# Optimization experiments

Hardware: AMD Instinct MI355X
Metric: run time of the kernel (lower is better)

## Reference

```python
import jax, jax.numpy as jnp
import numpy as np

N_NODES = 50000
N_EDGES = 800000
D_IN = 16


def gcn_conv(x, edge_index, W, b, n_nodes):
    """PyG GCNConv: x' = D^{-1/2} (A + I) D^{-1/2} X W + b (add_self_loops=True)."""
    h = x @ W  # [N, d_out] - transform before propagate (small d => cheaper)
    src = jnp.concatenate([edge_index[0], jnp.arange(n_nodes)])  # add self-loops
    dst = jnp.concatenate([edge_index[1], jnp.arange(n_nodes)])
    deg = jax.ops.segment_sum(jnp.ones_like(dst, dtype=h.dtype), dst,
                              num_segments=n_nodes)  # in-degree incl. self-loop
    deg_inv_sqrt = jnp.where(deg > 0, jax.lax.rsqrt(deg), 0.0)
    norm = deg_inv_sqrt[src] * deg_inv_sqrt[dst]  # [E+N]
    msg = h[src] * norm[:, None]                  # gather + scale
    out = jax.ops.segment_sum(msg, dst, num_segments=n_nodes)  # scatter-add
    return out + b


def setup_inputs() -> dict:
    key = jax.random.key(0)
    ks = jax.random.split(key, 16)
    d = D_IN
    x = jax.random.normal(ks[0], (N_NODES, d), dtype=jnp.float32)
    edge_index = jax.random.randint(ks[1], (2, N_EDGES), 0, N_NODES, dtype=jnp.int64)

    def glorot(k, fan_in, fan_out):
        s = (6.0 / (fan_in + fan_out)) ** 0.5
        return jax.random.uniform(k, (fan_in, fan_out), jnp.float32, -s, s)

    return {
        "x": x,
        "edge_index": edge_index,
        "W1": glorot(ks[2], d, 2 * d),      "b1": jnp.zeros((2 * d,), jnp.float32),
        "W2": glorot(ks[3], 2 * d, 4 * d),  "b2": jnp.zeros((4 * d,), jnp.float32),
        "W3": glorot(ks[4], 4 * d, 8 * d),  "b3": jnp.zeros((8 * d,), jnp.float32),
        "Wl1": glorot(ks[5], 8 * d, 4 * d), "bl1": jnp.zeros((4 * d,), jnp.float32),
        "Wl2": glorot(ks[6], 4 * d, 2 * d), "bl2": jnp.zeros((2 * d,), jnp.float32),
        "Wl3": glorot(ks[7], 2 * d, d),     "bl3": jnp.zeros((d,), jnp.float32),
    }


def reference(x, edge_index, W1, b1, W2, b2, W3, b3, Wl1, bl1, Wl2, bl2, Wl3, bl3):
    n = x.shape[0]
    # note: original applies relu twice per conv; relu is idempotent
    out = jax.nn.relu(gcn_conv(x, edge_index, W1, b1, n))
    out = jax.nn.relu(gcn_conv(out, edge_index, W2, b2, n))
    out = jax.nn.relu(gcn_conv(out, edge_index, W3, b3, n))
    out = jax.nn.relu(out @ Wl1 + bl1)
    out = jax.nn.relu(out @ Wl2 + bl2)
    out = jax.nn.relu(out @ Wl3 + bl3)
    return out
```

## Files before the change

### kernel.cpp

```cpp
#include <hip/hip_runtime.h>

#define TPB 256
#define TE  2048
#define MAXB 6144

typedef _Float16 half_t;
typedef _Float16 half4 __attribute__((ext_vector_type(4)));
typedef _Float16 half8 __attribute__((ext_vector_type(8)));
typedef float float8v __attribute__((ext_vector_type(8)));

static inline int cdiv(int a, int b) { return (a + b - 1) / b; }


__global__ void __launch_bounds__(TPB)
k_binscatter(const int* __restrict__ src, const int* __restrict__ dst,
             int* __restrict__ bcur, int* __restrict__ ncnt,
             unsigned int* __restrict__ gbuf, int e, int nb) {
    __shared__ int lcnt[256], loffs[256], lcur[256], gres[256];
    __shared__ int ss[256];
    __shared__ unsigned int ldata[TE];
    const int tid = threadIdx.x;
    const int base = blockIdx.x * TE;
    const int cnt = min(TE, e - base);
    lcnt[tid] = 0;
    __syncthreads();

    unsigned int myv[TE / TPB];
    int myb[TE / TPB];
#pragma unroll
    for (int k = 0; k < TE / TPB; ++k) {
        int j = tid + k * TPB;
        if (j < cnt) {
            int d = dst[base + j], s = src[base + j];
            int b = d >> 8;
            myv[k] = ((unsigned)b << 24) | ((unsigned)(d & 255) << 16) | (unsigned)s;
            myb[k] = b;
            atomicAdd(&lcnt[b], 1);
            atomicAdd(&ncnt[d], 1);
        } else myb[k] = -1;
    }
    __syncthreads();
    {
        int v = lcnt[tid];
        ss[tid] = v;
        __syncthreads();
        for (int d = 1; d < 256; d <<= 1) {
            int x2 = (tid >= d) ? ss[tid - d] : 0;
            __syncthreads();
            ss[tid] += x2;
            __syncthreads();
        }
        loffs[tid] = ss[tid] - v;
        lcur[tid] = ss[tid] - v;
    }
    __syncthreads();
    if (tid < nb && lcnt[tid])
        gres[tid] = tid * MAXB + atomicAdd(&bcur[tid], lcnt[tid]);
#pragma unroll
    for (int k = 0; k < TE / TPB; ++k) {
        if (myb[k] >= 0) {
            int p = atomicAdd(&lcur[myb[k]], 1);
            ldata[p] = myv[k];
        }
    }
    __syncthreads();
    for (int j = tid; j < cnt; j += TPB) {
        unsigned int v = ldata[j];
        int b = v >> 24;
        gbuf[gres[b] + (j - loffs[b])] = v & 0xFFFFFFu;
    }
}

__global__ void __launch_bounds__(TPB)
k_csr(const unsigned int* __restrict__ gbuf, const int* __restrict__ bcur,
      const int* __restrict__ ncnt, const float* __restrict__ x,
      int* __restrict__ offs, unsigned short* __restrict__ nch,
      float* __restrict__ dinv, unsigned short* __restrict__ ssrc,
      half_t* __restrict__ G, int n, int nb) {
    __shared__ int ss[256], lcur2[256];
    __shared__ float sdinv[256];
    __shared__ unsigned short stage[MAXB];
    const int b = blockIdx.x;
    const int t = threadIdx.x;
    const int s0 = b * MAXB;
    const int m = bcur[b];

    const int v = ncnt[b * 256 + t];
    const int pv = (v + 7) & ~7;
    ss[t] = pv;
    __syncthreads();
    for (int d = 1; d < 256; d <<= 1) {
        int x2 = (t >= d) ? ss[t - d] : 0;
        __syncthreads();
        ss[t] += x2;
        __syncthreads();
    }
    const int lo = ss[t] - pv;
    lcur2[t] = lo;
    float di = rsqrtf((float)v + 1.0f);
    sdinv[t] = di;
    int node = b * 256 + t;
    if (node < n) {
        offs[node] = s0 + lo;
        nch[node] = (unsigned short)(pv >> 3);
        dinv[node] = di;
    }
    __syncthreads();
    for (int j = t; j < m; j += TPB) {
        unsigned int u = gbuf[s0 + j];
        int p = atomicAdd(&lcur2[(u >> 16) & 255], 1);
        stage[p] = (unsigned short)(u & 0xFFFFu);
    }
    __syncthreads();
    for (int q = lo + v; q < lo + pv; ++q)
        stage[q] = (unsigned short)n;
    __syncthreads();
    const int tot = ss[255];
    for (int j = t; j < tot; j += TPB) ssrc[s0 + j] = stage[j];

    const int base = b * 256;
    const int cn = min(256, n - base);
    const float4* X4 = (const float4*)x;
    half4* G4 = (half4*)G;
    for (int j = t; j < cn * 4; j += TPB) {
        int nl = j >> 2, k4 = j & 3;
        float4 vv = X4[(size_t)(base + nl) * 4 + k4];
        float d = sdinv[nl];
        half4 h;
        h.x = (half_t)(vv.x * d); h.y = (half_t)(vv.y * d);
        h.z = (half_t)(vv.z * d); h.w = (half_t)(vv.w * d);
        G4[(size_t)(base + nl) * 4 + k4] = h;
    }
    if (b == 0 && t < 4) G4[(size_t)n * 4 + t] = half4{0, 0, 0, 0};
}

template<int DI, int DO, int R, bool SCALE, bool OUT_HALF, bool WHALF, bool ZSENT>
__global__ void __launch_bounds__(TPB, 4)
k_conv(const int* __restrict__ offs, const unsigned short* __restrict__ nch,
       const unsigned short* __restrict__ ssrc,
       const half_t* __restrict__ G, const float* __restrict__ dinv,
       const float* __restrict__ W, const float* __restrict__ b,
       void* __restrict__ outp, int n) {
    constexpr int CT = DO / 4;
    constexpr int RT = TPB / CT;
    constexpr int TM = RT * R;
    constexpr int K4 = DI / 4;
    constexpr int PX = K4 + 1;
    constexpr int C  = DI / 8;
    static_assert(TM * C == TPB, "gather/gemm tile mismatch");
    __shared__ float4 sW4[WHALF ? 1 : DI * CT];
    __shared__ half4  sWh[WHALF ? DI * CT : 1];
    __shared__ float4 sX4[TM * PX];
    __shared__ int soffs[TM];
    __shared__ unsigned short snch[TM];
    const int tid = threadIdx.x;
    const int r0 = blockIdx.x * TM;

    const float4* Wg = (const float4*)W;
    for (int t = tid; t < DI * CT; t += TPB) {
        float4 w = Wg[t];
        if (WHALF) {
            half4 h;
            h.x = (half_t)w.x; h.y = (half_t)w.y;
            h.z = (half_t)w.z; h.w = (half_t)w.w;
            sWh[t] = h;
        } else {
            sW4[t] = w;
        }
    }
    if (tid < TM) {
        int row = r0 + tid;
        soffs[tid] = (row < n) ? offs[row] : 0;
        snch[tid] = (row < n) ? nch[row] : (unsigned short)0;
    }
    __syncthreads();

    {
        int lrow = tid / C;
        int gc = tid - lrow * C;
        int row = r0 + lrow;
        float8v acc;
#pragma unroll
        for (int q = 0; q < 8; ++q) acc[q] = 0.f;
        if (row < n) {
            const half8* Grow = (const half8*)G;
            const unsigned gcU = (unsigned)gc;
            half8 hs = Grow[(unsigned)row * C + gcU];
#pragma unroll
            for (int q = 0; q < 8; ++q) acc[q] = (float)hs[q];
            const int nchunks = snch[lrow];
            const uint4* sv = (const uint4*)(ssrc + soffs[lrow]);
            int k = 0;
            for (; k + 2 <= nchunks; k += 2) {
                uint4 pa = sv[k];
                uint4 pb = sv[k + 1];
                unsigned a0 = pa.x & 0xFFFFu, a1 = pa.x >> 16;
                unsigned a2 = pa.y & 0xFFFFu, a3 = pa.y >> 16;
                unsigned a4 = pa.z & 0xFFFFu, a5 = pa.z >> 16;
                unsigned a6 = pa.w & 0xFFFFu, a7 = pa.w >> 16;
                unsigned b0 = pb.x & 0xFFFFu, b1 = pb.x >> 16;
                unsigned b2 = pb.y & 0xFFFFu, b3 = pb.y >> 16;
                unsigned b4 = pb.z & 0xFFFFu, b5 = pb.z >> 16;
                unsigned b6 = pb.w & 0xFFFFu, b7 = pb.w >> 16;
                half8 ga0 = Grow[a0 * C + gcU];
                half8 ga1 = Grow[a1 * C + gcU];
                half8 ga2 = Grow[a2 * C + gcU];
                half8 ga3 = Grow[a3 * C + gcU];
                half8 ga4 = Grow[a4 * C + gcU];
                half8 ga5 = Grow[a5 * C + gcU];
                half8 ga6 = Grow[a6 * C + gcU];
                half8 ga7 = Grow[a7 * C + gcU];
                half8 gb0 = Grow[b0 * C + gcU];
                half8 gb1 = Grow[b1 * C + gcU];
                half8 gb2 = Grow[b2 * C + gcU];
                half8 gb3 = Grow[b3 * C + gcU];
                half8 gb4 = Grow[b4 * C + gcU];
                half8 gb5 = Grow[b5 * C + gcU];
                half8 gb6 = Grow[b6 * C + gcU];
                half8 gb7 = Grow[b7 * C + gcU];
#pragma unroll
                for (int q = 0; q < 8; ++q)
                    acc[q] += (((((float)ga0[q] + (float)ga1[q]) + ((float)ga2[q] + (float)ga3[q]))
                             +  (((float)ga4[q] + (float)ga5[q]) + ((float)ga6[q] + (float)ga7[q])))
                             + ((((float)gb0[q] + (float)gb1[q]) + ((float)gb2[q] + (float)gb3[q]))
                             +  (((float)gb4[q] + (float)gb5[q]) + ((float)gb6[q] + (float)gb7[q]))));
            }
            if (k < nchunks) {
                uint4 pk = sv[k];
                unsigned a0 = pk.x & 0xFFFFu, a1 = pk.x >> 16;
                unsigned a2 = pk.y & 0xFFFFu, a3 = pk.y >> 16;
                unsigned a4 = pk.z & 0xFFFFu, a5 = pk.z >> 16;
                unsigned a6 = pk.w & 0xFFFFu, a7 = pk.w >> 16;
                half8 g0 = Grow[a0 * C + gcU];
                half8 g1 = Grow[a1 * C + gcU];
                half8 g2 = Grow[a2 * C + gcU];
                half8 g3 = Grow[a3 * C + gcU];
                half8 g4 = Grow[a4 * C + gcU];
                half8 g5 = Grow[a5 * C + gcU];
                half8 g6 = Grow[a6 * C + gcU];
                half8 g7 = Grow[a7 * C + gcU];
#pragma unroll
                for (int q = 0; q < 8; ++q)
                    acc[q] += (((float)g0[q] + (float)g1[q]) + ((float)g2[q] + (float)g3[q]))
                            + (((float)g4[q] + (float)g5[q]) + ((float)g6[q] + (float)g7[q]));
            }
            float di = dinv[row];
#pragma unroll
            for (int q = 0; q < 8; ++q) acc[q] *= di;
        }
        sX4[lrow * PX + 2 * gc]     = make_float4(acc[0], acc[1], acc[2], acc[3]);
        sX4[lrow * PX + 2 * gc + 1] = make_float4(acc[4], acc[5], acc[6], acc[7]);
    }
    __syncthreads();

    const int c = tid & (CT - 1);
    const int rg = tid / CT;
    const int rbase = rg * R;
    float4 acc[R];
#pragma unroll
    for (int r = 0; r < R; ++r) acc[r] = make_float4(0.f, 0.f, 0.f, 0.f);
#pragma unroll 2
    for (int k4 = 0; k4 < K4; ++k4) {
        float4 xv[R];
#pragma unroll
        for (int r = 0; r < R; ++r) xv[r] = sX4[(rbase + r) * PX + k4];
#pragma unroll
        for (int kk = 0; kk < 4; ++kk) {
            float4 wv;
            if (WHALF) {
                half4 wh = sWh[(k4 * 4 + kk) * CT + c];
                wv = make_float4((float)wh.x, (float)wh.y, (float)wh.z, (float)wh.w);
            } else {
                wv = sW4[(k4 * 4 + kk) * CT + c];
            }
#pragma unroll
            for (int r = 0; r < R; ++r) {
                float xs = (kk == 0) ? xv[r].x : (kk == 1) ? xv[r].y
                         : (kk == 2) ? xv[r].z : xv[r].w;
                acc[r].x += xs * wv.x; acc[r].y += xs * wv.y;
                acc[r].z += xs * wv.z; acc[r].w += xs * wv.w;
            }
        }
    }

    float4 bc = ((const float4*)b)[c];
#pragma unroll
    for (int r = 0; r < R; ++r) {
        int row = r0 + rbase + r;
        if (row < n) {
            float4 o;
            o.x = fmaxf(acc[r].x + bc.x, 0.f);
            o.y = fmaxf(acc[r].y + bc.y, 0.f);
            o.z = fmaxf(acc[r].z + bc.z, 0.f);
            o.w = fmaxf(acc[r].w + bc.w, 0.f);
            if (SCALE) {
                float d = dinv[row];
                o.x *= d; o.y *= d; o.z *= d; o.w *= d;
            }
            if (OUT_HALF) {
                half4 h;
                h.x = (half_t)o.x; h.y = (half_t)o.y;
                h.z = (half_t)o.z; h.w = (half_t)o.w;
                ((half4*)outp)[(size_t)row * CT + c] = h;
            } else {
                ((float4*)outp)[(size_t)row * CT + c] = o;
            }
        }
    }
    if (ZSENT && OUT_HALF && blockIdx.x == 0 && tid < CT)
        ((half4*)outp)[(size_t)n * CT + tid] = half4{0, 0, 0, 0};
}

__global__ void __launch_bounds__(TPB, 4)
k_conv3_head(const int* __restrict__ offs, const unsigned short* __restrict__ nch,
             const unsigned short* __restrict__ ssrc,
             const half_t* __restrict__ G, const float* __restrict__ dinv,
             const float* __restrict__ W, const float* __restrict__ b,
             const float* __restrict__ Wl1, const float* __restrict__ bl1,
             const float* __restrict__ Wl2, const float* __restrict__ bl2,
             const float* __restrict__ Wl3, const float* __restrict__ bl3,
             float* __restrict__ out, int n) {
    constexpr int DI = 64, DO = 128, R = 4;
    constexpr int CT = DO / 4;
    constexpr int TM = (TPB / CT) * R;
    constexpr int K4 = DI / 4;
    constexpr int PX = K4 + 1;
    constexpr int C  = DI / 8;
    constexpr int XP = 136;
    __shared__ union {
        struct { half4 sWh[DI * CT]; float4 sX4[TM * PX]; } g;
        struct { half_t X3[TM * XP]; half_t hW1[128 * 64];
                 float h1[TM * 65]; float h2[TM * 33]; } h;
    } S;
    __shared__ int soffs[TM];
    __shared__ unsigned short snch[TM];
    const int tid = threadIdx.x;
    const int r0 = blockIdx.x * TM;

    const float4* Wg = (const float4*)W;
    for (int t = tid; t < DI * CT; t += TPB) {
        float4 w = Wg[t];
        half4 hh;
        hh.x = (half_t)w.x; hh.y = (half_t)w.y;
        hh.z = (half_t)w.z; hh.w = (half_t)w.w;
        S.g.sWh[t] = hh;
    }
    if (tid < TM) {
        int row = r0 + tid;
        soffs[tid] = (row < n) ? offs[row] : 0;
        snch[tid] = (row < n) ? nch[row] : (unsigned short)0;
    }
    __syncthreads();

    {
        int lrow = tid / C;
        int gc = tid - lrow * C;
        int row = r0 + lrow;
        float8v acc;
#pragma unroll
        for (int q = 0; q < 8; ++q) acc[q] = 0.f;
        if (row < n) {
            const half8* Grow = (const half8*)G;
            const unsigned gcU = (unsigned)gc;
            half8 hs = Grow[(unsigned)row * C + gcU];
#pragma unroll
            for (int q = 0; q < 8; ++q) acc[q] = (float)hs[q];
            const int nchunks = snch[lrow];
            const uint4* sv = (const uint4*)(ssrc + soffs[lrow]);
            int k = 0;
            for (; k + 2 <= nchunks; k += 2) {
                uint4 pa = sv[k];
                uint4 pb = sv[k + 1];
                unsigned a0 = pa.x & 0xFFFFu, a1 = pa.x >> 16;
                unsigned a2 = pa.y & 0xFFFFu, a3 = pa.y >> 16;
                unsigned a4 = pa.z & 0xFFFFu, a5 = pa.z >> 16;
                unsigned a6 = pa.w & 0xFFFFu, a7 = pa.w >> 16;
                unsigned b0 = pb.x & 0xFFFFu, b1 = pb.x >> 16;
                unsigned b2 = pb.y & 0xFFFFu, b3 = pb.y >> 16;
                unsigned b4 = pb.z & 0xFFFFu, b5 = pb.z >> 16;
                unsigned b6 = pb.w & 0xFFFFu, b7 = pb.w >> 16;
                half8 ga0 = Grow[a0 * C + gcU];
                half8 ga1 = Grow[a1 * C + gcU];
                half8 ga2 = Grow[a2 * C + gcU];
                half8 ga3 = Grow[a3 * C + gcU];
                half8 ga4 = Grow[a4 * C + gcU];
                half8 ga5 = Grow[a5 * C + gcU];
                half8 ga6 = Grow[a6 * C + gcU];
                half8 ga7 = Grow[a7 * C + gcU];
                half8 gb0 = Grow[b0 * C + gcU];
                half8 gb1 = Grow[b1 * C + gcU];
                half8 gb2 = Grow[b2 * C + gcU];
                half8 gb3 = Grow[b3 * C + gcU];
                half8 gb4 = Grow[b4 * C + gcU];
                half8 gb5 = Grow[b5 * C + gcU];
                half8 gb6 = Grow[b6 * C + gcU];
                half8 gb7 = Grow[b7 * C + gcU];
#pragma unroll
                for (int q = 0; q < 8; ++q)
                    acc[q] += (((((float)ga0[q] + (float)ga1[q]) + ((float)ga2[q] + (float)ga3[q]))
                             +  (((float)ga4[q] + (float)ga5[q]) + ((float)ga6[q] + (float)ga7[q])))
                             + ((((float)gb0[q] + (float)gb1[q]) + ((float)gb2[q] + (float)gb3[q]))
                             +  (((float)gb4[q] + (float)gb5[q]) + ((float)gb6[q] + (float)gb7[q]))));
            }
            if (k < nchunks) {
                uint4 pk = sv[k];
                unsigned a0 = pk.x & 0xFFFFu, a1 = pk.x >> 16;
                unsigned a2 = pk.y & 0xFFFFu, a3 = pk.y >> 16;
                unsigned a4 = pk.z & 0xFFFFu, a5 = pk.z >> 16;
                unsigned a6 = pk.w & 0xFFFFu, a7 = pk.w >> 16;
                half8 g0 = Grow[a0 * C + gcU];
                half8 g1 = Grow[a1 * C + gcU];
                half8 g2 = Grow[a2 * C + gcU];
                half8 g3 = Grow[a3 * C + gcU];
                half8 g4 = Grow[a4 * C + gcU];
                half8 g5 = Grow[a5 * C + gcU];
                half8 g6 = Grow[a6 * C + gcU];
                half8 g7 = Grow[a7 * C + gcU];
#pragma unroll
                for (int q = 0; q < 8; ++q)
                    acc[q] += (((float)g0[q] + (float)g1[q]) + ((float)g2[q] + (float)g3[q]))
                            + (((float)g4[q] + (float)g5[q]) + ((float)g6[q] + (float)g7[q]));
            }
            float di = dinv[row];
#pragma unroll
            for (int q = 0; q < 8; ++q) acc[q] *= di;
        }
        S.g.sX4[lrow * PX + 2 * gc]     = make_float4(acc[0], acc[1], acc[2], acc[3]);
        S.g.sX4[lrow * PX + 2 * gc + 1] = make_float4(acc[4], acc[5], acc[6], acc[7]);
    }
    __syncthreads();

    const int c = tid & (CT - 1);
    const int rg = tid / CT;
    const int rbase = rg * R;
    float4 acc[R];
#pragma unroll
    for (int r = 0; r < R; ++r) acc[r] = make_float4(0.f, 0.f, 0.f, 0.f);
#pragma unroll 2
    for (int k4 = 0; k4 < K4; ++k4) {
        float4 xv[R];
#pragma unroll
        for (int r = 0; r < R; ++r) xv[r] = S.g.sX4[(rbase + r) * PX + k4];
#pragma unroll
        for (int kk = 0; kk < 4; ++kk) {
            half4 wh = S.g.sWh[(k4 * 4 + kk) * CT + c];
            float4 wv = make_float4((float)wh.x, (float)wh.y, (float)wh.z, (float)wh.w);
#pragma unroll
            for (int r = 0; r < R; ++r) {
                float xs = (kk == 0) ? xv[r].x : (kk == 1) ? xv[r].y
                         : (kk == 2) ? xv[r].z : xv[r].w;
                acc[r].x += xs * wv.x; acc[r].y += xs * wv.y;
                acc[r].z += xs * wv.z; acc[r].w += xs * wv.w;
            }
        }
    }
    {
        float4 bc = ((const float4*)b)[c];
#pragma unroll
        for (int r = 0; r < R; ++r) {
            acc[r].x = fmaxf(acc[r].x + bc.x, 0.f);
            acc[r].y = fmaxf(acc[r].y + bc.y, 0.f);
            acc[r].z = fmaxf(acc[r].z + bc.z, 0.f);
            acc[r].w = fmaxf(acc[r].w + bc.w, 0.f);
        }
    }
    __syncthreads();

#pragma unroll
    for (int r = 0; r < R; ++r) {
        half4 hv;
        hv.x = (half_t)acc[r].x; hv.y = (half_t)acc[r].y;
        hv.z = (half_t)acc[r].z; hv.w = (half_t)acc[r].w;
        *(half4*)&S.h.X3[(rbase + r) * XP + c * 4] = hv;
    }
    for (int t = tid; t < 128 * 64; t += TPB) S.h.hW1[t] = (half_t)Wl1[t];
    __syncthreads();

    {
        const int c4 = tid & 15;
        const int rowg = tid >> 4;
        float a1[2][4];
#pragma unroll
        for (int r = 0; r < 2; ++r)
#pragma unroll
            for (int j = 0; j < 4; ++j) a1[r][j] = 0.f;
        for (int k8 = 0; k8 < 16; ++k8) {
            half8 xh[2];
#pragma unroll
            for (int r = 0; r < 2; ++r)
                xh[r] = *(const half8*)&S.h.X3[(rowg * 2 + r) * XP + k8 * 8];
#pragma unroll
            for (int q = 0; q < 8; ++q) {
                int k = k8 * 8 + q;
                half4 w = *(const half4*)&S.h.hW1[k * 64 + c4 * 4];
                float w0 = (float)w.x, w1 = (float)w.y, w2 = (float)w.z, w3 = (float)w.w;
#pragma unroll
                for (int r = 0; r < 2; ++r) {
                    float xs = (float)xh[r][q];
                    a1[r][0] += xs * w0; a1[r][1] += xs * w1;
                    a1[r][2] += xs * w2; a1[r][3] += xs * w3;
                }
            }
        }
        float4 bc = ((const float4*)bl1)[c4];
#pragma unroll
        for (int r = 0; r < 2; ++r) {
            int rl = rowg * 2 + r;
            S.h.h1[rl * 65 + c4 * 4 + 0] = fmaxf(a1[r][0] + bc.x, 0.f);
            S.h.h1[rl * 65 + c4 * 4 + 1] = fmaxf(a1[r][1] + bc.y, 0.f);
            S.h.h1[rl * 65 + c4 * 4 + 2] = fmaxf(a1[r][2] + bc.z, 0.f);
            S.h.h1[rl * 65 + c4 * 4 + 3] = fmaxf(a1[r][3] + bc.w, 0.f);
        }
    }
    __syncthreads();

    {
        const int c4 = tid & 7;
        const int rl = tid >> 3;
        float a2[4] = {0.f, 0.f, 0.f, 0.f};
#pragma unroll 4
        for (int k = 0; k < 64; ++k) {
            float4 w = ((const float4*)Wl2)[k * 8 + c4];
            float xs = S.h.h1[rl * 65 + k];
            a2[0] += xs * w.x; a2[1] += xs * w.y;
            a2[2] += xs * w.z; a2[3] += xs * w.w;
        }
        float4 bc = ((const float4*)bl2)[c4];
        S.h.h2[rl * 33 + c4 * 4 + 0] = fmaxf(a2[0] + bc.x, 0.f);
        S.h.h2[rl * 33 + c4 * 4 + 1] = fmaxf(a2[1] + bc.y, 0.f);
        S.h.h2[rl * 33 + c4 * 4 + 2] = fmaxf(a2[2] + bc.z, 0.f);
        S.h.h2[rl * 33 + c4 * 4 + 3] = fmaxf(a2[3] + bc.w, 0.f);
    }
    __syncthreads();

    {
        const int c4 = tid & 3;
        const int rl = tid >> 2;
        if (rl < TM) {
            float s0 = 0.f, s1 = 0.f, s2 = 0.f, s3 = 0.f;
#pragma unroll 4
            for (int k = 0; k < 32; ++k) {
                float4 w = ((const float4*)Wl3)[k * 4 + c4];
                float xs = S.h.h2[rl * 33 + k];
                s0 += xs * w.x; s1 += xs * w.y;
                s2 += xs * w.z; s3 += xs * w.w;
            }
            int row = r0 + rl;
            if (row < n) {
                float4 bc = ((const float4*)bl3)[c4];
                float4 o;
                o.x = fmaxf(s0 + bc.x, 0.f);
                o.y = fmaxf(s1 + bc.y, 0.f);
                o.z = fmaxf(s2 + bc.z, 0.f);
                o.w = fmaxf(s3 + bc.w, 0.f);
                ((float4*)out)[(size_t)row * 4 + c4] = o;
            }
        }
    }
}

extern "C" void kernel_launch(void* const* d_in, const int* in_sizes, int n_in,
                              void* d_out, int out_size, void* d_ws, size_t ws_size,
                              hipStream_t stream) {
    const float* x   = (const float*)d_in[0];
    const int*   ei  = (const int*)d_in[1];
    const float* W1  = (const float*)d_in[2];
    const float* bb1 = (const float*)d_in[3];
    const float* W2  = (const float*)d_in[4];
    const float* bb2 = (const float*)d_in[5];
    const float* W3  = (const float*)d_in[6];
    const float* bb3 = (const float*)d_in[7];
    const float* Wl1 = (const float*)d_in[8];
    const float* bl1 = (const float*)d_in[9];
    const float* Wl2 = (const float*)d_in[10];
    const float* bl2 = (const float*)d_in[11];
    const float* Wl3 = (const float*)d_in[12];
    const float* bl3 = (const float*)d_in[13];
    float* out = (float*)d_out;

    const int n = in_sizes[0] / 16;
    const int e = in_sizes[1] / 2;
    const int* src = ei;
    const int* dst = ei + e;
    const int nb = cdiv(n, 256);

    char* p = (char*)d_ws;
    auto alloc = [&](size_t bytes) {
        char* r = p;
        p += (bytes + 255) & ~(size_t)255;
        return r;
    };
    int*            bcur = (int*)           alloc(1024);
    int*            ncnt = (int*)           alloc((size_t)nb * 256 * 4);
    float*          dinv = (float*)         alloc((size_t)n * 4);
    int*            offs = (int*)           alloc((size_t)n * 4);
    unsigned short* nch  = (unsigned short*)alloc((size_t)n * 2);
    unsigned int*   gbuf = (unsigned int*)  alloc((size_t)nb * MAXB * 4);
    unsigned short* ssrc = (unsigned short*)alloc((size_t)nb * MAXB * 2);
    half_t*         H1   = (half_t*)        alloc((size_t)(n + 1) * 64 * 2);
    half_t*         H2   = (half_t*)        alloc((size_t)(n + 1) * 32 * 2);

    hipMemsetAsync(bcur, 0, 1024 + (size_t)nb * 256 * 4, stream);
    k_binscatter<<<cdiv(e, TE), TPB, 0, stream>>>(src, dst, bcur, ncnt, gbuf, e, nb);
    k_csr<<<nb, TPB, 0, stream>>>(gbuf, bcur, ncnt, x, offs, nch, dinv, ssrc, H1, n, nb);

    k_conv<16, 32, 4, true, true, false, true><<<cdiv(n, 128), TPB, 0, stream>>>(
        offs, nch, ssrc, H1, dinv, W1, bb1, H2, n);
    k_conv<32, 64, 4, true, true, false, true><<<cdiv(n, 64), TPB, 0, stream>>>(
        offs, nch, ssrc, H2, dinv, W2, bb2, H1, n);
    k_conv3_head<<<cdiv(n, 32), TPB, 0, stream>>>(
        offs, nch, ssrc, H1, dinv, W3, bb3, Wl1, bl1, Wl2, bl2, Wl3, bl3, out, n);
}
```

Baseline: 218.2 us.

## Use MFMA f16 matrix cores for conv3 transform and first head layer

Replaces the scalar FMA dense products in the fused conv3+head kernel (the 64->128 conv3 weight multiply and the 128->64 Wl1 layer) with 16x16x32 f16 MFMA instructions. Weights are transposed into padded shared-memory tiles and the aggregated features are stored as f16. The kernel now handles 32 rows per block instead of 32 with the old R scheme. The aim is to cut ALU time in the head. It adds a transpose-on-load with scattered 16-bit shared stores, and rounds the conv3 inputs to f16 before the multiply.

```diff
diff --git a/kernel.cpp b/kernel.cpp
--- a/kernel.cpp
+++ b/kernel.cpp
@@ -8,6 +8,7 @@
 typedef _Float16 half4 __attribute__((ext_vector_type(4)));
 typedef _Float16 half8 __attribute__((ext_vector_type(8)));
 typedef float float8v __attribute__((ext_vector_type(8)));
+typedef float f32x4 __attribute__((ext_vector_type(4)));
 
 static inline int cdiv(int a, int b) { return (a + b - 1) / b; }
 
@@ -320,30 +321,34 @@
              const float* __restrict__ Wl2, const float* __restrict__ bl2,
              const float* __restrict__ Wl3, const float* __restrict__ bl3,
              float* __restrict__ out, int n) {
-    constexpr int DI = 64, DO = 128, R = 4;
-    constexpr int CT = DO / 4;
-    constexpr int TM = (TPB / CT) * R;
-    constexpr int K4 = DI / 4;
-    constexpr int PX = K4 + 1;
-    constexpr int C  = DI / 8;
-    constexpr int XP = 136;
-    __shared__ union {
-        struct { half4 sWh[DI * CT]; float4 sX4[TM * PX]; } g;
-        struct { half_t X3[TM * XP]; half_t hW1[128 * 64];
+    constexpr int TM = 32;
+    constexpr int C  = 8;
+    constexpr int XPA = 72;
+    constexpr int XPB = 136;
+    __shared__ __align__(16) union {
+        struct { half_t sWhT[128 * XPA]; half_t X16[TM * XPA]; } g;
+        struct { half_t X3[TM * XPB]; half_t sW1T[64 * XPB];
                  float h1[TM * 65]; float h2[TM * 33]; } h;
     } S;
     __shared__ int soffs[TM];
     __shared__ unsigned short snch[TM];
     const int tid = threadIdx.x;
     const int r0 = blockIdx.x * TM;
-
-    const float4* Wg = (const float4*)W;
-    for (int t = tid; t < DI * CT; t += TPB) {
-        float4 w = Wg[t];
-        half4 hh;
-        hh.x = (half_t)w.x; hh.y = (half_t)w.y;
-        hh.z = (half_t)w.z; hh.w = (half_t)w.w;
-        S.g.sWh[t] = hh;
+    const int lane = tid & 63;
+    const int wv = tid >> 6;
+    const int lr = lane & 15;
+    const int kq = lane >> 4;
+
+    {
+        const float4* Wg = (const float4*)W;
+        for (int t = tid; t < 64 * 32; t += TPB) {
+            int k = t >> 5, c4 = t & 31;
+            float4 w = Wg[t];
+            S.g.sWhT[(c4 * 4 + 0) * XPA + k] = (half_t)w.x;
+            S.g.sWhT[(c4 * 4 + 1) * XPA + k] = (half_t)w.y;
+            S.g.sWhT[(c4 * 4 + 2) * XPA + k] = (half_t)w.z;
+            S.g.sWhT[(c4 * 4 + 3) * XPA + k] = (half_t)w.w;
+        }
     }
     if (tid < TM) {
         int row = r0 + tid;
@@ -425,92 +430,76 @@
 #pragma unroll
             for (int q = 0; q < 8; ++q) acc[q] *= di;
         }
-        S.g.sX4[lrow * PX + 2 * gc]     = make_float4(acc[0], acc[1], acc[2], acc[3]);
-        S.g.sX4[lrow * PX + 2 * gc + 1] = make_float4(acc[4], acc[5], acc[6], acc[7]);
-    }
-    __syncthreads();
-
-    const int c = tid & (CT - 1);
-    const int rg = tid / CT;
-    const int rbase = rg * R;
-    float4 acc[R];
-#pragma unroll
-    for (int r = 0; r < R; ++r) acc[r] = make_float4(0.f, 0.f, 0.f, 0.f);
-#pragma unroll 2
-    for (int k4 = 0; k4 < K4; ++k4) {
-        float4 xv[R];
-#pragma unroll
-        for (int r = 0; r < R; ++r) xv[r] = S.g.sX4[(rbase + r) * PX + k4];
-#pragma unroll
-        for (int kk = 0; kk < 4; ++kk) {
-            half4 wh = S.g.sWh[(k4 * 4 + kk) * CT + c];
-            float4 wv = make_float4((float)wh.x, (float)wh.y, (float)wh.z, (float)wh.w);
-#pragma unroll
-            for (int r = 0; r < R; ++r) {
-                float xs = (kk == 0) ? xv[r].x : (kk == 1) ? xv[r].y
-                         : (kk == 2) ? xv[r].z : xv[r].w;
-                acc[r].x += xs * wv.x; acc[r].y += xs * wv.y;
-                acc[r].z += xs * wv.z; acc[r].w += xs * wv.w;
-            }
-        }
-    }
-    {
-        float4 bc = ((const float4*)b)[c];
-#pragma unroll
-        for (int r = 0; r < R; ++r) {
-            acc[r].x = fmaxf(acc[r].x + bc.x, 0.f);
-            acc[r].y = fmaxf(acc[r].y + bc.y, 0.f);
-            acc[r].z = fmaxf(acc[r].z + bc.z, 0.f);
-            acc[r].w = fmaxf(acc[r].w + bc.w, 0.f);
-        }
-    }
-    __syncthreads();
-
-#pragma unroll
-    for (int r = 0; r < R; ++r) {
-        half4 hv;
-        hv.x = (half_t)acc[r].x; hv.y = (half_t)acc[r].y;
-        hv.z = (half_t)acc[r].z; hv.w = (half_t)acc[r].w;
-        *(half4*)&S.h.X3[(rbase + r) * XP + c * 4] = hv;
-    }
-    for (int t = tid; t < 128 * 64; t += TPB) S.h.hW1[t] = (half_t)Wl1[t];
-    __syncthreads();
-
-    {
-        const int c4 = tid & 15;
-        const int rowg = tid >> 4;
-        float a1[2][4];
-#pragma unroll
-        for (int r = 0; r < 2; ++r)
-#pragma unroll
-            for (int j = 0; j < 4; ++j) a1[r][j] = 0.f;
-        for (int k8 = 0; k8 < 16; ++k8) {
-            half8 xh[2];
-#pragma unroll
-            for (int r = 0; r < 2; ++r)
-                xh[r] = *(const half8*)&S.h.X3[(rowg * 2 + r) * XP + k8 * 8];
-#pragma unroll
-            for (int q = 0; q < 8; ++q) {
-                int k = k8 * 8 + q;
-                half4 w = *(const half4*)&S.h.hW1[k * 64 + c4 * 4];
-                float w0 = (float)w.x, w1 = (float)w.y, w2 = (float)w.z, w3 = (float)w.w;
-#pragma unroll
-                for (int r = 0; r < 2; ++r) {
-                    float xs = (float)xh[r][q];
-                    a1[r][0] += xs * w0; a1[r][1] += xs * w1;
-                    a1[r][2] += xs * w2; a1[r][3] += xs * w3;
-                }
-            }
-        }
-        float4 bc = ((const float4*)bl1)[c4];
-#pragma unroll
-        for (int r = 0; r < 2; ++r) {
-            int rl = rowg * 2 + r;
-            S.h.h1[rl * 65 + c4 * 4 + 0] = fmaxf(a1[r][0] + bc.x, 0.f);
-            S.h.h1[rl * 65 + c4 * 4 + 1] = fmaxf(a1[r][1] + bc.y, 0.f);
-            S.h.h1[rl * 65 + c4 * 4 + 2] = fmaxf(a1[r][2] + bc.z, 0.f);
-            S.h.h1[rl * 65 + c4 * 4 + 3] = fmaxf(a1[r][3] + bc.w, 0.f);
-        }
+        half8 hv;
+#pragma unroll
+        for (int q = 0; q < 8; ++q) hv[q] = (half_t)acc[q];
+        *(half8*)&S.g.X16[lrow * XPA + gc * 8] = hv;
+    }
+    __syncthreads();
+
+    f32x4 acc3[2][2];
+#pragma unroll
+    for (int mt = 0; mt < 2; ++mt)
+#pragma unroll
+        for (int nt = 0; nt < 2; ++nt) acc3[mt][nt] = f32x4{0.f, 0.f, 0.f, 0.f};
+#pragma unroll
+    for (int ks = 0; ks < 2; ++ks) {
+        half8 a0 = *(const half8*)&S.g.X16[lr * XPA + ks * 32 + kq * 8];
+        half8 a1 = *(const half8*)&S.g.X16[(lr + 16) * XPA + ks * 32 + kq * 8];
+        half8 b0 = *(const half8*)&S.g.sWhT[(wv * 32 + lr) * XPA + ks * 32 + kq * 8];
+        half8 b1 = *(const half8*)&S.g.sWhT[(wv * 32 + 16 + lr) * XPA + ks * 32 + kq * 8];
+        acc3[0][0] = __builtin_amdgcn_mfma_f32_16x16x32_f16(a0, b0, acc3[0][0], 0, 0, 0);
+        acc3[0][1] = __builtin_amdgcn_mfma_f32_16x16x32_f16(a0, b1, acc3[0][1], 0, 0, 0);
+        acc3[1][0] = __builtin_amdgcn_mfma_f32_16x16x32_f16(a1, b0, acc3[1][0], 0, 0, 0);
+        acc3[1][1] = __builtin_amdgcn_mfma_f32_16x16x32_f16(a1, b1, acc3[1][1], 0, 0, 0);
+    }
+    const float bc30 = b[wv * 32 + lr];
+    const float bc31 = b[wv * 32 + 16 + lr];
+    __syncthreads();
+
+#pragma unroll
+    for (int mt = 0; mt < 2; ++mt)
+#pragma unroll
+        for (int nt = 0; nt < 2; ++nt) {
+            float bb = nt ? bc31 : bc30;
+#pragma unroll
+            for (int j = 0; j < 4; ++j) {
+                float v = fmaxf(acc3[mt][nt][j] + bb, 0.f);
+                S.h.X3[(mt * 16 + kq * 4 + j) * XPB + wv * 32 + nt * 16 + lr] = (half_t)v;
+            }
+        }
+    {
+        const float4* W1g = (const float4*)Wl1;
+        for (int t = tid; t < 128 * 16; t += TPB) {
+            int k = t >> 4, c4 = t & 15;
+            float4 w = W1g[t];
+            S.h.sW1T[(c4 * 4 + 0) * XPB + k] = (half_t)w.x;
+            S.h.sW1T[(c4 * 4 + 1) * XPB + k] = (half_t)w.y;
+            S.h.sW1T[(c4 * 4 + 2) * XPB + k] = (half_t)w.z;
+            S.h.sW1T[(c4 * 4 + 3) * XPB + k] = (half_t)w.w;
+        }
+    }
+    __syncthreads();
+
+    f32x4 h1a[2];
+    h1a[0] = f32x4{0.f, 0.f, 0.f, 0.f};
+    h1a[1] = f32x4{0.f, 0.f, 0.f, 0.f};
+#pragma unroll
+    for (int ks = 0; ks < 4; ++ks) {
+        half8 a0 = *(const half8*)&S.h.X3[lr * XPB + ks * 32 + kq * 8];
+        half8 a1 = *(const half8*)&S.h.X3[(lr + 16) * XPB + ks * 32 + kq * 8];
+        half8 bb = *(const half8*)&S.h.sW1T[(wv * 16 + lr) * XPB + ks * 32 + kq * 8];
+        h1a[0] = __builtin_amdgcn_mfma_f32_16x16x32_f16(a0, bb, h1a[0], 0, 0, 0);
+        h1a[1] = __builtin_amdgcn_mfma_f32_16x16x32_f16(a1, bb, h1a[1], 0, 0, 0);
+    }
+    {
+        float bb = bl1[wv * 16 + lr];
+#pragma unroll
+        for (int mt = 0; mt < 2; ++mt)
+#pragma unroll
+            for (int j = 0; j < 4; ++j)
+                S.h.h1[(mt * 16 + kq * 4 + j) * 65 + wv * 16 + lr] =
+                    fmaxf(h1a[mt][j] + bb, 0.f);
     }
     __syncthreads();
 
```

New measurement: 204.3 us. 6.4% less time.
